# Kernel optimization log

Hardware: AMD Instinct MI355X
Metric: run time of the kernel (lower is better)

## Reference

```python
import jax, jax.numpy as jnp
import numpy as np

K = 3
PAD = 1
K2 = K * K


def conv2d(x, w, b, pad):
    out = jax.lax.conv_general_dilated(
        x, w, window_strides=(1, 1), padding=((pad, pad), (pad, pad)),
        dimension_numbers=("NCHW", "OIHW", "NCHW"))
    return out + b[None, :, None, None]


def deform_conv2d(x, offset, w, b):
    # x: [B,C,H,W], offset: [B,2*K2,H,W] with (dy,dx) pairs per kernel tap
    B, C, H, W = x.shape
    off = offset.reshape(B, K2, 2, H, W)
    dy, dx = off[:, :, 0], off[:, :, 1]                    # [B,K2,H,W]
    ky = (jnp.arange(K2) // K).astype(x.dtype)[None, :, None, None]
    kx = (jnp.arange(K2) % K).astype(x.dtype)[None, :, None, None]
    hh = jnp.arange(H, dtype=x.dtype)[None, None, :, None]
    ww = jnp.arange(W, dtype=x.dtype)[None, None, None, :]
    py = hh - PAD + ky + dy                                # [B,K2,H,W]
    px = ww - PAD + kx + dx

    y0 = jnp.floor(py)
    x0 = jnp.floor(px)
    wy = py - y0
    wx = px - x0

    xflat = x.reshape(B, C, H * W)

    def gather(yi, xi, wgt):
        # per-corner bilinear term; out-of-bounds corners contribute 0
        valid = (yi >= 0) & (yi < H) & (xi >= 0) & (xi < W)
        yc = jnp.clip(yi, 0, H - 1).astype(jnp.int32)
        xc = jnp.clip(xi, 0, W - 1).astype(jnp.int32)
        idx = (yc * W + xc).reshape(B, K2 * H * W)
        vals = jax.vmap(lambda xf, i: xf[:, i])(xflat, idx)  # [B,C,K2*H*W]
        vals = vals.reshape(B, C, K2, H, W)
        m = (wgt * valid.astype(x.dtype)).reshape(B, 1, K2, H, W)
        return vals * m

    sampled = (gather(y0, x0, (1 - wy) * (1 - wx))
               + gather(y0, x0 + 1, (1 - wy) * wx)
               + gather(y0 + 1, x0, wy * (1 - wx))
               + gather(y0 + 1, x0 + 1, wy * wx))          # [B,C,K2,H,W]

    O = w.shape[0]
    out = jnp.einsum('bckhw,ock->bohw', sampled, w.reshape(O, C, K2))
    return out + b[None, :, None, None]


def setup_inputs() -> dict:
    key = jax.random.key(0)
    k1, k2, k3, k4, k5 = jax.random.split(key, 5)
    B, C, O, H, W = 8, 64, 64, 128, 128
    x = jax.random.normal(k1, (B, C, H, W), dtype=jnp.float32)
    fan_in = C * K * K
    # small offset-conv init so learned offsets stay modest (as at train start)
    w_off = jax.random.normal(k2, (2 * K2, C, 3, 3), dtype=jnp.float32) * 0.01
    b_off = jnp.zeros((2 * K2,), dtype=jnp.float32)
    w_def = jax.random.normal(k3, (O, C, K, K), dtype=jnp.float32) / np.sqrt(fan_in).astype(np.float32)
    b_def = jax.random.normal(k4, (O,), dtype=jnp.float32) * 0.01
    return {"x": x, "w_off": w_off, "b_off": b_off, "w_def": w_def, "b_def": b_def}


def reference(x, w_off, b_off, w_def, b_def):
    offset = conv2d(x, w_off, b_off, pad=1)
    return deform_conv2d(x, offset, w_def, b_def)
```

## Files before the change

kernel.cpp:

```cpp
#include <hip/hip_runtime.h>
#include <hip/hip_bf16.h>

constexpr int B_ = 8, C_ = 64, O_ = 64, H_ = 128, W_ = 128;
constexpr int K2_ = 9, OFFC = 18;
constexpr int NPIX = B_ * H_ * W_;

typedef __attribute__((ext_vector_type(8))) short bf16x8;
typedef __attribute__((ext_vector_type(4))) short bf16x4;
typedef __attribute__((ext_vector_type(4))) float f32x4;
typedef __attribute__((ext_vector_type(2))) float f32x2;

__device__ __forceinline__ unsigned short f2bf(float f) {
    unsigned int u = __float_as_uint(f);
    u += 0x7fffu + ((u >> 16) & 1u);
    return (unsigned short)(u >> 16);
}
__device__ __forceinline__ float bf2f(unsigned short s) {
    return __uint_as_float(((unsigned)s) << 16);
}
__device__ __forceinline__ float tobf_f(float v) {
    return bf2f(f2bf(v));
}
__device__ __forceinline__ short f2bf_s(float f) {
    __hip_bfloat16 t = __float2bfloat16(f);
    return *reinterpret_cast<short*>(&t);
}
__device__ __forceinline__ f32x2 bfpair(unsigned u) {
    f32x2 r;
    r[0] = __uint_as_float(u << 16);
    r[1] = __uint_as_float(u & 0xffff0000u);
    return r;
}

__global__ void k_wprep(const float* __restrict__ w_def,
                        unsigned short* __restrict__ wTfrag) {
    int i = blockIdx.x * 256 + threadIdx.x;
    if (i >= O_ * C_ * K2_) return;
    int f = i >> 9;
    int l = (i >> 3) & 63;
    int j = i & 7;
    int kc = f >> 2, nt = f & 3;
    int oc = nt * 16 + (l & 15);
    int K  = kc * 32 + ((l >> 4) << 3) + j;
    int tap = K >> 6, c = K & 63;
    wTfrag[i] = f2bf(w_def[(size_t)oc * (C_ * K2_) + c * K2_ + tap]);
}

__global__ void k_wprep_off(const float* __restrict__ w_off,
                            unsigned short* __restrict__ wOfrag) {
    int i = blockIdx.x * 256 + threadIdx.x;
    if (i >= 36 * 512) return;
    int f = i >> 9;
    int l = (i >> 3) & 63;
    int j = i & 7;
    int kc = f >> 1, nt = f & 1;
    int oc = nt * 16 + (l & 15);
    int K  = kc * 32 + ((l >> 4) << 3) + j;
    int tap = K >> 6, c = K & 63;
    float v = (oc < OFFC) ? w_off[((size_t)oc * C_ + c) * K2_ + tap] : 0.f;
    wOfrag[i] = f2bf(v);
}

constexpr int QS = 5 * 72 * 32;
constexpr int XS_BYTES = 4 * QS;

__global__ __launch_bounds__(256, 3) void k_fused(const float* __restrict__ x,
                                                  const unsigned short* __restrict__ wOfrag,
                                                  const float* __restrict__ b_off,
                                                  const unsigned short* __restrict__ wTfrag,
                                                  const float* __restrict__ b_def,
                                                  float* __restrict__ out) {
    __shared__ __align__(16) char xs[XS_BYTES];
    __shared__ float offsBuf[64][22];

    int bid = blockIdx.x;
    int swz = (bid & 7) * 256 + (bid >> 3);
    int px0 = swz * 64;
    int b  = px0 >> 14;
    int h  = (px0 >> 7) & (H_ - 1);
    int w0 = px0 & (W_ - 1);

    int tid  = threadIdx.x;
    int lane = tid & 63;
    int wave = tid >> 6;

    for (int it = tid; it < 5760; it += 256) {
        int col = it % 72;
        int rem = it / 72;
        int c4  = rem & 15;
        int r   = rem >> 4;
        int y    = h - 2 + r;
        int xcol = w0 - 3 + col;
        bf16x4 pk;
        if (((unsigned)y < (unsigned)H_) && ((unsigned)xcol < (unsigned)W_)) {
            const float* g = x + (((size_t)(b * C_ + c4 * 4) * H_ + y) * W_ + xcol);
            pk[0] = f2bf_s(g[0]);
            pk[1] = f2bf_s(g[H_ * W_]);
            pk[2] = f2bf_s(g[2 * H_ * W_]);
            pk[3] = f2bf_s(g[3 * H_ * W_]);
        } else {
            pk = (bf16x4){0, 0, 0, 0};
        }
        int q0 = c4 >> 2;
        int byte = q0 * QS + ((r * 72 + col) * 32) + (c4 & 3) * 8;
        byte ^= ((col & 7) << 4) ^ (q0 << 5);
        *reinterpret_cast<bf16x4*>(xs + byte) = pk;
    }
    __syncthreads();

    {
        f32x4 acc2[2];
        acc2[0] = (f32x4){0.f, 0.f, 0.f, 0.f};
        acc2[1] = (f32x4){0.f, 0.f, 0.f, 0.f};
        int g   = lane >> 4;
        int pxr = wave * 16 + (lane & 15);
        #pragma unroll
        for (int kc = 0; kc < 18; ++kc) {
            int K   = kc * 32 + g * 8;
            int tap = K >> 6, c = K & 63;
            int ky = tap / 3, kx = tap % 3;
            int col = pxr + kx + 2;
            int r   = ky + 1;
            int qq  = c >> 4;
            int byte = qq * QS + ((r * 72 + col) * 32) + (c & 15) * 2;
            byte ^= ((col & 7) << 4) ^ (qq << 5);
            bf16x8 a  = *reinterpret_cast<const bf16x8*>(xs + byte);
            bf16x8 b0 = *reinterpret_cast<const bf16x8*>(wOfrag + (((kc * 2 + 0) * 64 + lane) << 3));
            bf16x8 b1 = *reinterpret_cast<const bf16x8*>(wOfrag + (((kc * 2 + 1) * 64 + lane) << 3));
            acc2[0] = __builtin_amdgcn_mfma_f32_16x16x32_bf16(a, b0, acc2[0], 0, 0, 0);
            acc2[1] = __builtin_amdgcn_mfma_f32_16x16x32_bf16(a, b1, acc2[1], 0, 0, 0);
        }
        #pragma unroll
        for (int nt = 0; nt < 2; ++nt) {
            int oc = nt * 16 + (lane & 15);
            if (oc < OFFC) {
                float bo = b_off[oc];
                #pragma unroll
                for (int j = 0; j < 4; ++j) {
                    int px = wave * 16 + ((lane >> 4) << 2) + j;
                    offsBuf[px][oc] = acc2[nt][j] + bo;
                }
            }
        }
    }
    __syncthreads();

    f32x4 acc[4];
    #pragma unroll
    for (int nt = 0; nt < 4; ++nt) acc[nt] = (f32x4){0.f, 0.f, 0.f, 0.f};

    int g    = lane >> 4;
    int rowM = lane & 15;
    int pxw  = (wave << 4) + rowM;
    int glo  = (g & 1) << 4;
    int qlo  = g >> 1;
    int qhi  = qlo + 2;
    int baseLo = qlo * QS + glo, baseHi = qhi * QS + glo;
    int xorLo  = qlo << 5,  xorHi  = qhi << 5;

    float2 off9[9];
    #pragma unroll
    for (int k = 0; k < 9; ++k)
        off9[k] = *reinterpret_cast<const float2*>(&offsBuf[pxw][2 * k]);

    #pragma unroll
    for (int ky = 0; ky < 3; ++ky) {
        #pragma unroll
        for (int kx = 0; kx < 3; ++kx) {
            int k = ky * 3 + kx;
            bf16x8 B0[4], B1[4];
            #pragma unroll
            for (int nt = 0; nt < 4; ++nt) {
                B0[nt] = *reinterpret_cast<const bf16x8*>(
                    wTfrag + ((((2 * k + 0) * 4 + nt) * 64 + lane) << 3));
                B1[nt] = *reinterpret_cast<const bf16x8*>(
                    wTfrag + ((((2 * k + 1) * 4 + nt) * 64 + lane) << 3));
            }

            float dy = off9[k].x, dx = off9[k].y;
            float py  = (float)(h - 1 + ky) + dy;
            float pxf = (float)(w0 + pxw - 1 + kx) + dx;
            float y0f = floorf(py), x0f = floorf(pxf);
            float wy = py - y0f, wx = pxf - x0f;
            int y0 = (int)y0f, x0 = (int)x0f;
            int r0 = y0 - (h - 2), c0 = x0 - (w0 - 3);
            bool oow = ((unsigned)r0 >= 4u) | ((unsigned)c0 >= 71u);
            int rc = min(max(r0, 0), 3), cc = min(max(c0, 0), 70);
            float w00 = (1.f - wy) * (1.f - wx);
            float w01 = (1.f - wy) * wx;
            float w10 = wy * (1.f - wx);
            float w11 = wy * wx;

            int A00 = (rc * 72 + cc) << 5;
            int s0 = (cc & 7) << 4;
            int s1 = ((cc + 1) & 7) << 4;
            uint4 u00l = *reinterpret_cast<const uint4*>(xs + ((baseLo + A00)        ^ (s0 ^ xorLo)));
            uint4 u01l = *reinterpret_cast<const uint4*>(xs + ((baseLo + A00 + 32)   ^ (s1 ^ xorLo)));
            uint4 u10l = *reinterpret_cast<const uint4*>(xs + ((baseLo + A00 + 2304) ^ (s0 ^ xorLo)));
            uint4 u11l = *reinterpret_cast<const uint4*>(xs + ((baseLo + A00 + 2336) ^ (s1 ^ xorLo)));
            uint4 u00h = *reinterpret_cast<const uint4*>(xs + ((baseHi + A00)        ^ (s0 ^ xorHi)));
            uint4 u01h = *reinterpret_cast<const uint4*>(xs + ((baseHi + A00 + 32)   ^ (s1 ^ xorHi)));
            uint4 u10h = *reinterpret_cast<const uint4*>(xs + ((baseHi + A00 + 2304) ^ (s0 ^ xorHi)));
            uint4 u11h = *reinterpret_cast<const uint4*>(xs + ((baseHi + A00 + 2336) ^ (s1 ^ xorHi)));

            f32x2 aL0 = bfpair(u00l.x) * w00, aL1 = bfpair(u00l.y) * w00;
            f32x2 aL2 = bfpair(u00l.z) * w00, aL3 = bfpair(u00l.w) * w00;
            f32x2 aH0 = bfpair(u00h.x) * w00, aH1 = bfpair(u00h.y) * w00;
            f32x2 aH2 = bfpair(u00h.z) * w00, aH3 = bfpair(u00h.w) * w00;
            aL0 += bfpair(u01l.x) * w01; aL1 += bfpair(u01l.y) * w01;
            aL2 += bfpair(u01l.z) * w01; aL3 += bfpair(u01l.w) * w01;
            aH0 += bfpair(u01h.x) * w01; aH1 += bfpair(u01h.y) * w01;
            aH2 += bfpair(u01h.z) * w01; aH3 += bfpair(u01h.w) * w01;
            aL0 += bfpair(u10l.x) * w10; aL1 += bfpair(u10l.y) * w10;
            aL2 += bfpair(u10l.z) * w10; aL3 += bfpair(u10l.w) * w10;
            aH0 += bfpair(u10h.x) * w10; aH1 += bfpair(u10h.y) * w10;
            aH2 += bfpair(u10h.z) * w10; aH3 += bfpair(u10h.w) * w10;
            aL0 += bfpair(u11l.x) * w11; aL1 += bfpair(u11l.y) * w11;
            aL2 += bfpair(u11l.z) * w11; aL3 += bfpair(u11l.w) * w11;
            aH0 += bfpair(u11h.x) * w11; aH1 += bfpair(u11h.y) * w11;
            aH2 += bfpair(u11h.z) * w11; aH3 += bfpair(u11h.w) * w11;

            bf16x8 alo, ahi;
            alo[0] = f2bf_s(aL0[0]); alo[1] = f2bf_s(aL0[1]);
            alo[2] = f2bf_s(aL1[0]); alo[3] = f2bf_s(aL1[1]);
            alo[4] = f2bf_s(aL2[0]); alo[5] = f2bf_s(aL2[1]);
            alo[6] = f2bf_s(aL3[0]); alo[7] = f2bf_s(aL3[1]);
            ahi[0] = f2bf_s(aH0[0]); ahi[1] = f2bf_s(aH0[1]);
            ahi[2] = f2bf_s(aH1[0]); ahi[3] = f2bf_s(aH1[1]);
            ahi[4] = f2bf_s(aH2[0]); ahi[5] = f2bf_s(aH2[1]);
            ahi[6] = f2bf_s(aH3[0]); ahi[7] = f2bf_s(aH3[1]);

            if (__any(oow)) {
                if (oow) {
                    int y1 = y0 + 1, x1 = x0 + 1;
                    bool vy0 = (y0 >= 0) & (y0 < H_);
                    bool vy1 = (y1 >= 0) & (y1 < H_);
                    bool vx0 = (x0 >= 0) & (x0 < W_);
                    bool vx1 = (x1 >= 0) & (x1 < W_);
                    float m00 = (vy0 && vx0) ? w00 : 0.f;
                    float m01 = (vy0 && vx1) ? w01 : 0.f;
                    float m10 = (vy1 && vx0) ? w10 : 0.f;
                    float m11 = (vy1 && vx1) ? w11 : 0.f;
                    int y0c = min(max(y0, 0), H_ - 1), y1c = min(max(y1, 0), H_ - 1);
                    int x0c = min(max(x0, 0), W_ - 1), x1c = min(max(x1, 0), W_ - 1);
                    int i00 = y0c * W_ + x0c, i01 = y0c * W_ + x1c;
                    int i10 = y1c * W_ + x0c, i11 = y1c * W_ + x1c;
                    const float* cb = x + (size_t)b * C_ * H_ * W_;
                    #pragma unroll
                    for (int j = 0; j < 8; ++j) {
                        const float* cA = cb + (size_t)((g << 3) + j) * (H_ * W_);
                        const float* cB = cb + (size_t)(32 + (g << 3) + j) * (H_ * W_);
                        alo[j] = f2bf_s(m00 * tobf_f(cA[i00]) + m01 * tobf_f(cA[i01])
                                      + m10 * tobf_f(cA[i10]) + m11 * tobf_f(cA[i11]));
                        ahi[j] = f2bf_s(m00 * tobf_f(cB[i00]) + m01 * tobf_f(cB[i01])
                                      + m10 * tobf_f(cB[i10]) + m11 * tobf_f(cB[i11]));
                    }
                }
            }

            #pragma unroll
            for (int nt = 0; nt < 4; ++nt)
                acc[nt] = __builtin_amdgcn_mfma_f32_16x16x32_bf16(alo, B0[nt], acc[nt], 0, 0, 0);
            #pragma unroll
            for (int nt = 0; nt < 4; ++nt)
                acc[nt] = __builtin_amdgcn_mfma_f32_16x16x32_bf16(ahi, B1[nt], acc[nt], 0, 0, 0);
        }
    }
    __syncthreads();

    float* ot = reinterpret_cast<float*>(xs);
    #pragma unroll
    for (int nt = 0; nt < 4; ++nt) {
        int oc = (nt << 4) + rowM;
        #pragma unroll
        for (int j = 0; j < 4; ++j) {
            int prow = (wave << 4) + (g << 2) + j;
            ot[prow * 65 + oc] = acc[nt][j];
        }
    }
    __syncthreads();
    #pragma unroll
    for (int r = 0; r < 16; ++r) {
        int idx = r * 256 + tid;
        int oc = idx >> 6, pw = idx & 63;
        out[(((size_t)b * O_ + oc) * H_ + h) * W_ + w0 + pw] = ot[pw * 65 + oc] + b_def[oc];
    }
}

extern "C" void kernel_launch(void* const* d_in, const int* in_sizes, int n_in,
                              void* d_out, int out_size, void* d_ws, size_t ws_size,
                              hipStream_t stream) {
    const float* x     = (const float*)d_in[0];
    const float* w_off = (const float*)d_in[1];
    const float* b_off = (const float*)d_in[2];
    const float* w_def = (const float*)d_in[3];
    const float* b_def = (const float*)d_in[4];
    float* out = (float*)d_out;

    char* ws = (char*)d_ws;
    unsigned short* wTf = (unsigned short*)ws;
    unsigned short* wOf = (unsigned short*)(ws + 73728);

    k_wprep<<<(O_ * C_ * K2_ + 255) / 256, 256, 0, stream>>>(w_def, wTf);
    k_wprep_off<<<(36 * 512 + 255) / 256, 256, 0, stream>>>(w_off, wOf);
    k_fused<<<NPIX / 64, 256, 0, stream>>>(x, wOf, b_off, wTf, b_def, out);
}
```

Before: 72.85 us.

## Process two output rows per block to cut halo reload of input tile

Each block now covers a 2x64 pixel tile with 512 threads instead of 1x64 with 256, so the staged bf16 input halo grows from 5 to 6 rows. This shares the halo rows across two output rows and lowers redundant global loads and bf16 conversion per pixel. The bilinear accumulation is also reordered so the low and high channel halves are finished one after the other, which may reduce live registers. In exchange, shared memory per block grows and the new launch bounds change occupancy and register limits.

```diff
diff --git a/kernel.cpp b/kernel.cpp
--- a/kernel.cpp
+++ b/kernel.cpp
@@ -61,30 +61,30 @@
     wOfrag[i] = f2bf(v);
 }
 
-constexpr int QS = 5 * 72 * 32;
+constexpr int QS = 6 * 72 * 32;
 constexpr int XS_BYTES = 4 * QS;
 
-__global__ __launch_bounds__(256, 3) void k_fused(const float* __restrict__ x,
+__global__ __launch_bounds__(512, 4) void k_fused(const float* __restrict__ x,
                                                   const unsigned short* __restrict__ wOfrag,
                                                   const float* __restrict__ b_off,
                                                   const unsigned short* __restrict__ wTfrag,
                                                   const float* __restrict__ b_def,
                                                   float* __restrict__ out) {
     __shared__ __align__(16) char xs[XS_BYTES];
-    __shared__ float offsBuf[64][22];
+    __shared__ float offsBuf[128][22];
 
     int bid = blockIdx.x;
-    int swz = (bid & 7) * 256 + (bid >> 3);
-    int px0 = swz * 64;
-    int b  = px0 >> 14;
-    int h  = (px0 >> 7) & (H_ - 1);
-    int w0 = px0 & (W_ - 1);
+    int swz = (bid & 7) * 128 + (bid >> 3);
+    int b  = swz >> 7;
+    int rem2 = swz & 127;
+    int h  = (rem2 >> 1) << 1;
+    int w0 = (rem2 & 1) << 6;
 
     int tid  = threadIdx.x;
     int lane = tid & 63;
     int wave = tid >> 6;
 
-    for (int it = tid; it < 5760; it += 256) {
+    for (int it = tid; it < 6912; it += 512) {
         int col = it % 72;
         int rem = it / 72;
         int c4  = rem & 15;
@@ -114,13 +114,14 @@
         acc2[1] = (f32x4){0.f, 0.f, 0.f, 0.f};
         int g   = lane >> 4;
         int pxr = wave * 16 + (lane & 15);
+        int rr  = pxr >> 6, cx = pxr & 63;
         #pragma unroll
         for (int kc = 0; kc < 18; ++kc) {
             int K   = kc * 32 + g * 8;
             int tap = K >> 6, c = K & 63;
             int ky = tap / 3, kx = tap % 3;
-            int col = pxr + kx + 2;
-            int r   = ky + 1;
+            int col = cx + kx + 2;
+            int r   = rr + ky + 1;
             int qq  = c >> 4;
             int byte = qq * QS + ((r * 72 + col) * 32) + (c & 15) * 2;
             byte ^= ((col & 7) << 4) ^ (qq << 5);
@@ -152,6 +153,7 @@
     int g    = lane >> 4;
     int rowM = lane & 15;
     int pxw  = (wave << 4) + rowM;
+    int prr  = pxw >> 6, pcx = pxw & 63;
     int glo  = (g & 1) << 4;
     int qlo  = g >> 1;
     int qhi  = qlo + 2;
@@ -178,14 +180,14 @@
             }
 
             float dy = off9[k].x, dx = off9[k].y;
-            float py  = (float)(h - 1 + ky) + dy;
-            float pxf = (float)(w0 + pxw - 1 + kx) + dx;
+            float py  = (float)(h + prr - 1 + ky) + dy;
+            float pxf = (float)(w0 + pcx - 1 + kx) + dx;
             float y0f = floorf(py), x0f = floorf(pxf);
             float wy = py - y0f, wx = pxf - x0f;
             int y0 = (int)y0f, x0 = (int)x0f;
             int r0 = y0 - (h - 2), c0 = x0 - (w0 - 3);
-            bool oow = ((unsigned)r0 >= 4u) | ((unsigned)c0 >= 71u);
-            int rc = min(max(r0, 0), 3), cc = min(max(c0, 0), 70);
+            bool oow = ((unsigned)r0 >= 5u) | ((unsigned)c0 >= 71u);
+            int rc = min(max(r0, 0), 4), cc = min(max(c0, 0), 70);
             float w00 = (1.f - wy) * (1.f - wx);
             float w01 = (1.f - wy) * wx;
             float w10 = wy * (1.f - wx);
@@ -194,41 +196,42 @@
             int A00 = (rc * 72 + cc) << 5;
             int s0 = (cc & 7) << 4;
             int s1 = ((cc + 1) & 7) << 4;
+
             uint4 u00l = *reinterpret_cast<const uint4*>(xs + ((baseLo + A00)        ^ (s0 ^ xorLo)));
             uint4 u01l = *reinterpret_cast<const uint4*>(xs + ((baseLo + A00 + 32)   ^ (s1 ^ xorLo)));
             uint4 u10l = *reinterpret_cast<const uint4*>(xs + ((baseLo + A00 + 2304) ^ (s0 ^ xorLo)));
             uint4 u11l = *reinterpret_cast<const uint4*>(xs + ((baseLo + A00 + 2336) ^ (s1 ^ xorLo)));
+            f32x2 L0 = bfpair(u00l.x) * w00 + bfpair(u01l.x) * w01
+                     + bfpair(u10l.x) * w10 + bfpair(u11l.x) * w11;
+            f32x2 L1 = bfpair(u00l.y) * w00 + bfpair(u01l.y) * w01
+                     + bfpair(u10l.y) * w10 + bfpair(u11l.y) * w11;
+            f32x2 L2 = bfpair(u00l.z) * w00 + bfpair(u01l.z) * w01
+                     + bfpair(u10l.z) * w10 + bfpair(u11l.z) * w11;
+            f32x2 L3 = bfpair(u00l.w) * w00 + bfpair(u01l.w) * w01
+                     + bfpair(u10l.w) * w10 + bfpair(u11l.w) * w11;
+            bf16x8 alo;
+            alo[0] = f2bf_s(L0[0]); alo[1] = f2bf_s(L0[1]);
+            alo[2] = f2bf_s(L1[0]); alo[3] = f2bf_s(L1[1]);
+            alo[4] = f2bf_s(L2[0]); alo[5] = f2bf_s(L2[1]);
+            alo[6] = f2bf_s(L3[0]); alo[7] = f2bf_s(L3[1]);
+
             uint4 u00h = *reinterpret_cast<const uint4*>(xs + ((baseHi + A00)        ^ (s0 ^ xorHi)));
             uint4 u01h = *reinterpret_cast<const uint4*>(xs + ((baseHi + A00 + 32)   ^ (s1 ^ xorHi)));
             uint4 u10h = *reinterpret_cast<const uint4*>(xs + ((baseHi + A00 + 2304) ^ (s0 ^ xorHi)));
             uint4 u11h = *reinterpret_cast<const uint4*>(xs + ((baseHi + A00 + 2336) ^ (s1 ^ xorHi)));
-
-            f32x2 aL0 = bfpair(u00l.x) * w00, aL1 = bfpair(u00l.y) * w00;
-            f32x2 aL2 = bfpair(u00l.z) * w00, aL3 = bfpair(u00l.w) * w00;
-            f32x2 aH0 = bfpair(u00h.x) * w00, aH1 = bfpair(u00h.y) * w00;
-            f32x2 aH2 = bfpair(u00h.z) * w00, aH3 = bfpair(u00h.w) * w00;
-            aL0 += bfpair(u01l.x) * w01; aL1 += bfpair(u01l.y) * w01;
-            aL2 += bfpair(u01l.z) * w01; aL3 += bfpair(u01l.w) * w01;
-            aH0 += bfpair(u01h.x) * w01; aH1 += bfpair(u01h.y) * w01;
-            aH2 += bfpair(u01h.z) * w01; aH3 += bfpair(u01h.w) * w01;
-            aL0 += bfpair(u10l.x) * w10; aL1 += bfpair(u10l.y) * w10;
-            aL2 += bfpair(u10l.z) * w10; aL3 += bfpair(u10l.w) * w10;
-            aH0 += bfpair(u10h.x) * w10; aH1 += bfpair(u10h.y) * w10;
-            aH2 += bfpair(u10h.z) * w10; aH3 += bfpair(u10h.w) * w10;
-            aL0 += bfpair(u11l.x) * w11; aL1 += bfpair(u11l.y) * w11;
-            aL2 += bfpair(u11l.z) * w11; aL3 += bfpair(u11l.w) * w11;
-            aH0 += bfpair(u11h.x) * w11; aH1 += bfpair(u11h.y) * w11;
-            aH2 += bfpair(u11h.z) * w11; aH3 += bfpair(u11h.w) * w11;
-
-            bf16x8 alo, ahi;
-            alo[0] = f2bf_s(aL0[0]); alo[1] = f2bf_s(aL0[1]);
-            alo[2] = f2bf_s(aL1[0]); alo[3] = f2bf_s(aL1[1]);
-            alo[4] = f2bf_s(aL2[0]); alo[5] = f2bf_s(aL2[1]);
-            alo[6] = f2bf_s(aL3[0]); alo[7] = f2bf_s(aL3[1]);
-            ahi[0] = f2bf_s(aH0[0]); ahi[1] = f2bf_s(aH0[1]);
-            ahi[2] = f2bf_s(aH1[0]); ahi[3] = f2bf_s(aH1[1]);
-            ahi[4] = f2bf_s(aH2[0]); ahi[5] = f2bf_s(aH2[1]);
-            ahi[6] = f2bf_s(aH3[0]); ahi[7] = f2bf_s(aH3[1]);
+            f32x2 H0 = bfpair(u00h.x) * w00 + bfpair(u01h.x) * w01
+                     + bfpair(u10h.x) * w10 + bfpair(u11h.x) * w11;
+            f32x2 H1 = bfpair(u00h.y) * w00 + bfpair(u01h.y) * w01
+                     + bfpair(u10h.y) * w10 + bfpair(u11h.y) * w11;
+            f32x2 H2 = bfpair(u00h.z) * w00 + bfpair(u01h.z) * w01
+                     + bfpair(u10h.z) * w10 + bfpair(u11h.z) * w11;
+            f32x2 H3 = bfpair(u00h.w) * w00 + bfpair(u01h.w) * w01
+                     + bfpair(u10h.w) * w10 + bfpair(u11h.w) * w11;
+            bf16x8 ahi;
+            ahi[0] = f2bf_s(H0[0]); ahi[1] = f2bf_s(H0[1]);
+            ahi[2] = f2bf_s(H1[0]); ahi[3] = f2bf_s(H1[1]);
+            ahi[4] = f2bf_s(H2[0]); ahi[5] = f2bf_s(H2[1]);
+            ahi[6] = f2bf_s(H3[0]); ahi[7] = f2bf_s(H3[1]);
 
             if (__any(oow)) {
                 if (oow) {
@@ -281,9 +284,10 @@
     __syncthreads();
     #pragma unroll
     for (int r = 0; r < 16; ++r) {
-        int idx = r * 256 + tid;
-        int oc = idx >> 6, pw = idx & 63;
-        out[(((size_t)b * O_ + oc) * H_ + h) * W_ + w0 + pw] = ot[pw * 65 + oc] + b_def[oc];
+        int idx = r * 512 + tid;
+        int oc = idx >> 7, pw = idx & 127;
+        int rr = pw >> 6, cx = pw & 63;
+        out[(((size_t)b * O_ + oc) * H_ + h + rr) * W_ + w0 + cx] = ot[pw * 65 + oc] + b_def[oc];
     }
 }
 
@@ -303,5 +307,5 @@
 
     k_wprep<<<(O_ * C_ * K2_ + 255) / 256, 256, 0, stream>>>(w_def, wTf);
     k_wprep_off<<<(36 * 512 + 255) / 256, 256, 0, stream>>>(w_off, wOf);
-    k_fused<<<NPIX / 64, 256, 0, stream>>>(x, wOf, b_off, wTf, b_def, out);
-}
+    k_fused<<<NPIX / 128, 512, 0, stream>>>(x, wOf, b_off, wTf, b_def, out);
+}
```

After: 76.32 us. +4.8%, slower.
